# Performance work log

Hardware: AMD Instinct MI355X
Metric: run time of the kernel (lower is better)

Reference implementation:

```python
import jax, jax.numpy as jnp
import numpy as np

N, E, G = 50000, 600000, 512   # nodes, edges, graphs
F, D, L = 128, 128, 3          # in_features, hidden dim, num_gc_layers
ED = D * L                      # embedding_dim (readout='concat')
C = 1.0                         # curvature
MIN_NORM = 1e-15
BALL_EPS = 4e-3                 # hgcn PoincareBall proj eps for float32


def _logmap0(p, c):
    sc = jnp.sqrt(c)
    n = jnp.clip(jnp.linalg.norm(p, axis=-1, keepdims=True), MIN_NORM, None)
    return p / (sc * n) * jnp.arctanh(jnp.clip(sc * n, -1 + 1e-15, 1 - 1e-15))


def _expmap0(u, c):
    sc = jnp.sqrt(c)
    n = jnp.clip(jnp.linalg.norm(u, axis=-1, keepdims=True), MIN_NORM, None)
    return jnp.tanh(sc * n) * u / (sc * n)


def _proj(x, c):
    n = jnp.clip(jnp.linalg.norm(x, axis=-1, keepdims=True), MIN_NORM, None)
    maxn = (1.0 - BALL_EPS) / jnp.sqrt(c)
    return jnp.where(n > maxn, x / n * maxn, x)


def _gcn(x, W, b, src, dst):
    h = x @ W
    deg = jax.ops.segment_sum(jnp.ones_like(dst, dtype=h.dtype), dst, num_segments=N) + 1.0
    dinv = deg ** -0.5
    msg = h[src] * (dinv[src] * dinv[dst])[:, None]           # [E, D]
    agg = jax.ops.segment_sum(msg, dst, num_segments=N) + h * (dinv * dinv)[:, None]
    return agg + b


def _encoder(x, Ws, bs, src, dst, batch):
    xs = []
    for W, b in zip(Ws, bs):
        x = jax.nn.relu(_gcn(x, W, b, src, dst))
        xs.append(x)
    # readout='concat' with global_add_pool
    g = jnp.concatenate([jax.ops.segment_sum(h, batch, num_segments=G) for h in xs], axis=1)
    return g, jnp.concatenate(xs, axis=1)


def _mlp(x, W1, W2):  # proj_head: Linear (no bias), ReLU, Linear (no bias)
    return jax.nn.relu(x @ W1) @ W2


def setup_inputs() -> dict:
    key = jax.random.key(0)
    ks = jax.random.split(key, 24)

    def xav(k, i, o):
        return jax.random.normal(k, (i, o), dtype=jnp.float32) * np.float32(np.sqrt(2.0 / (i + o)))

    inp = {
        'x':   jax.random.normal(ks[0], (N, F), dtype=jnp.float32) * 1e-3,  # points inside the ball
        'x_s': jax.random.normal(ks[1], (N, F), dtype=jnp.float32) * 1e-3,
        'src': jax.random.randint(ks[2], (E,), 0, N, dtype=jnp.int32),
        'dst': jax.random.randint(ks[3], (E,), 0, N, dtype=jnp.int32),
        'batch': jnp.sort(jax.random.randint(ks[4], (N,), 0, G, dtype=jnp.int32)),
        # feature-branch GCN encoder
        'Wf0': xav(ks[5], F, D), 'Wf1': xav(ks[6], D, D), 'Wf2': xav(ks[7], D, D),
        'bf0': jnp.zeros((D,), jnp.float32), 'bf1': jnp.zeros((D,), jnp.float32), 'bf2': jnp.zeros((D,), jnp.float32),
        # structure-branch GCN encoder
        'Ws0': xav(ks[8], F, D), 'Ws1': xav(ks[9], D, D), 'Ws2': xav(ks[10], D, D),
        'bs0': jnp.zeros((D,), jnp.float32), 'bs1': jnp.zeros((D,), jnp.float32), 'bs2': jnp.zeros((D,), jnp.float32),
        # proj heads (biases removed by init_emb)
        'P1': xav(ks[11], ED, ED), 'P2': xav(ks[12], ED, ED),
        'G1': xav(ks[13], 2 * ED, ED), 'G2': xav(ks[14], ED, ED),
    }
    return inp


def reference(x, x_s, Wf0, Wf1, Wf2, bf0, bf1, bf2, Ws0, Ws1, Ws2, bs0, bs1, bs2, P1, P2, G1, G2, src, dst, batch):
    xt_f = _logmap0(x, C)
    xt_s = _logmap0(x_s, C)
    g_f, n_f = _encoder(xt_f, (Wf0, Wf1, Wf2), (bf0, bf1, bf2), src, dst, batch)
    g_s, n_s = _encoder(xt_s, (Ws0, Ws1, Ws2), (bs0, bs1, bs2), src, dst, batch)
    g = _mlp(jnp.concatenate((g_f, g_s), axis=1), G1, G2)
    e = lambda t: _proj(_expmap0(t, C), C)
    return (e(g), e(_mlp(g_f, P1, P2)), e(_mlp(n_f, P1, P2)), e(_mlp(g_s, P1, P2)), e(_mlp(n_s, P1, P2)))
```

## Files before the change

### kernel.cpp

```cpp
#include <hip/hip_runtime.h>
#include <math.h>

#define N_NODES 50000
#define N_EDGES 600000
#define N_GRAPHS 512
#define F_IN 128
#define D_HID 128
#define EDIM 384
#define M_ALL (N_NODES + N_GRAPHS)

typedef __attribute__((ext_vector_type(8))) short bf16x8;
typedef __attribute__((ext_vector_type(4))) float f32x4;
typedef __attribute__((ext_vector_type(16))) float f32x16;

static __device__ __forceinline__ float wave_reduce_sum(float s) {
#pragma unroll
  for (int off = 32; off > 0; off >>= 1) s += __shfl_xor(s, off, 64);
  return s;
}

static __device__ __forceinline__ int wave_reduce_sum_i(int s) {
#pragma unroll
  for (int off = 32; off > 0; off >>= 1) s += __shfl_xor(s, off, 64);
  return s;
}

static __device__ __forceinline__ short f2b(float f) {
  unsigned u = __float_as_uint(f);
  unsigned r = (u + 0x7FFFu + ((u >> 16) & 1u)) >> 16;
  return (short)r;
}

static __device__ __forceinline__ float b2f(short s) {
  return __uint_as_float(((unsigned)(unsigned short)s) << 16);
}


#define SCAN_BS 256
#define SCAN_NB ((N_NODES + SCAN_BS - 1) / SCAN_BS)

__global__ __launch_bounds__(SCAN_BS) void init_kernel(const int* __restrict__ batch,
                                                       int* __restrict__ cnt,
                                                       int* __restrict__ gptr) {
  int i = blockIdx.x * SCAN_BS + threadIdx.x;
  if (i < N_NODES) cnt[i] = 0;
  if (i <= N_GRAPHS) {
    int lo = 0, hi = N_NODES;
    while (lo < hi) { int mid = (lo + hi) >> 1; if (batch[mid] < i) lo = mid + 1; else hi = mid; }
    gptr[i] = lo;
  }
}

__global__ void hist_kernel(const int* __restrict__ dst, int* __restrict__ cnt) {
  int i = blockIdx.x * blockDim.x + threadIdx.x;
  if (i < N_EDGES) atomicAdd(&cnt[dst[i]], 1);
}

__global__ __launch_bounds__(SCAN_BS) void scan1_kernel(const int* __restrict__ cnt,
                                                        int* __restrict__ row_ptr,
                                                        int* __restrict__ bsum) {
  __shared__ int wsum[4];
  int tid = threadIdx.x, lane = tid & 63, wid = tid >> 6;
  int idx = blockIdx.x * SCAN_BS + tid;
  int v = (idx < N_NODES) ? cnt[idx] : 0;
  int x = v;
#pragma unroll
  for (int off = 1; off < 64; off <<= 1) {
    int t = __shfl_up(x, off, 64);
    if (lane >= off) x += t;
  }
  if (lane == 63) wsum[wid] = x;
  __syncthreads();
  int pre = 0, tot = 0;
#pragma unroll
  for (int w = 0; w < 4; ++w) { int s = wsum[w]; tot += s; if (w < wid) pre += s; }
  if (idx < N_NODES) row_ptr[idx + 1] = x + pre;
  if (tid == 0) bsum[blockIdx.x] = tot;
}

__global__ __launch_bounds__(SCAN_BS) void scan3_kernel(const int* __restrict__ cnt,
                                                        const int* __restrict__ bsum,
                                                        int* __restrict__ row_ptr,
                                                        int* __restrict__ cursor,
                                                        float* __restrict__ dinv) {
  __shared__ int ws[4];
  int tid = threadIdx.x, lane = tid & 63, wid = tid >> 6;
  int v = 0;
  if (tid < SCAN_NB && tid < blockIdx.x) v = bsum[tid];
  v = wave_reduce_sum_i(v);
  if (lane == 0) ws[wid] = v;
  __syncthreads();
  int boff = ws[0] + ws[1] + ws[2] + ws[3];
  int idx = blockIdx.x * SCAN_BS + tid;
  if (idx >= N_NODES) return;
  int val = row_ptr[idx + 1] + boff;
  row_ptr[idx + 1] = val;
  int c = cnt[idx];
  cursor[idx] = val - c;
  dinv[idx] = 1.0f / sqrtf((float)(c + 1));
  if (idx == 0) row_ptr[0] = 0;
}

__global__ void scatter_kernel(const int* __restrict__ src, const int* __restrict__ dst,
                               const float* __restrict__ dinv, int* __restrict__ cursor,
                               int* __restrict__ col, float* __restrict__ ew) {
  int e = blockIdx.x * blockDim.x + threadIdx.x;
  if (e >= N_EDGES) return;
  int s = src[e], d = dst[e];
  int pos = atomicAdd(&cursor[d], 1);
  col[pos] = s;
  ew[pos] = dinv[s] * dinv[d];
}


struct WcSeg { const float* W; short* Wt; int K; int Nc; };
struct WcArgs { WcSeg seg[10]; };

__global__ void wconv_all_kernel(WcArgs a) {
  int sidx = blockIdx.y;
  WcSeg s = a.seg[sidx];
  int i = blockIdx.x * blockDim.x + threadIdx.x;
  if (i >= s.K * s.Nc) return;
  int k = i / s.Nc, n = i - k * s.Nc;
  s.Wt[(size_t)n * s.K + k] = f2b(s.W[i]);
}


__global__ __launch_bounds__(256) void logmap2_kernel(const float* __restrict__ x,
                                                      const float* __restrict__ x_s,
                                                      short* __restrict__ Ab) {
  int w = blockIdx.x * 4 + (threadIdx.x >> 6);
  int lane = threadIdx.x & 63;
  if (w >= 2 * N_NODES) return;
  int br = (w >= N_NODES) ? 1 : 0;
  int row = br ? (w - N_NODES) : w;
  const float* xr = (br ? x_s : x) + (size_t)row * F_IN;
  float2 v = *(const float2*)(xr + lane * 2);
  float s = wave_reduce_sum(v.x * v.x + v.y * v.y);
  float n = sqrtf(s);
  float nc = fmaxf(n, 1e-15f);
  float f = atanhf(fminf(nc, 0.9999999f)) / nc;
  short2 o; o.x = f2b(v.x * f); o.y = f2b(v.y * f);
  *(short2*)(Ab + (size_t)row * 256 + br * 128 + lane * 2) = o;
}


__global__ __launch_bounds__(256) void agg2_kernel(const short* __restrict__ Xin, int lda,
                                                   const float* __restrict__ dinv,
                                                   const int* __restrict__ row_ptr,
                                                   const int* __restrict__ col,
                                                   const float* __restrict__ ew,
                                                   short* __restrict__ Xa) {
  int node = blockIdx.x * 4 + (threadIdx.x >> 6);
  int lane = threadIdx.x & 63;
  if (node >= N_NODES) return;
  float di = dinv[node];
  float wsf = di * di;
  short4 sv = *(const short4*)(Xin + (size_t)node * lda + lane * 4);
  float a0 = b2f(sv.x) * wsf, a1 = b2f(sv.y) * wsf, a2 = b2f(sv.z) * wsf, a3 = b2f(sv.w) * wsf;
  int s = row_ptr[node], e = row_ptr[node + 1];
  int j = s;
  for (; j + 4 <= e; j += 4) {
    int c0 = col[j], c1 = col[j + 1], c2 = col[j + 2], c3 = col[j + 3];
    float w0 = ew[j], w1 = ew[j + 1], w2 = ew[j + 2], w3 = ew[j + 3];
    short4 v0 = *(const short4*)(Xin + (size_t)c0 * lda + lane * 4);
    short4 v1 = *(const short4*)(Xin + (size_t)c1 * lda + lane * 4);
    short4 v2 = *(const short4*)(Xin + (size_t)c2 * lda + lane * 4);
    short4 v3 = *(const short4*)(Xin + (size_t)c3 * lda + lane * 4);
    a0 += b2f(v0.x) * w0; a1 += b2f(v0.y) * w0; a2 += b2f(v0.z) * w0; a3 += b2f(v0.w) * w0;
    a0 += b2f(v1.x) * w1; a1 += b2f(v1.y) * w1; a2 += b2f(v1.z) * w1; a3 += b2f(v1.w) * w1;
    a0 += b2f(v2.x) * w2; a1 += b2f(v2.y) * w2; a2 += b2f(v2.z) * w2; a3 += b2f(v2.w) * w2;
    a0 += b2f(v3.x) * w3; a1 += b2f(v3.y) * w3; a2 += b2f(v3.z) * w3; a3 += b2f(v3.w) * w3;
  }
  for (; j < e; ++j) {
    float w0 = ew[j];
    short4 v0 = *(const short4*)(Xin + (size_t)col[j] * lda + lane * 4);
    a0 += b2f(v0.x) * w0; a1 += b2f(v0.y) * w0; a2 += b2f(v0.z) * w0; a3 += b2f(v0.w) * w0;
  }
  short4 o; o.x = f2b(a0); o.y = f2b(a1); o.z = f2b(a2); o.w = f2b(a3);
  *(short4*)(Xa + (size_t)node * 256 + lane * 4) = o;
}


#define LDK 40

struct GemmZArgs {
  const short* A[2];
  const short* Bt[2];
  const float* bias[2];
  short* Cb[2];
  int lda, ldc, M, Nc, K, kexp, do_relu;
};

__global__ __launch_bounds__(256) void mfma_gemmz_kernel(GemmZArgs g) {
  __shared__ __align__(16) short As[128 * LDK];
  __shared__ __align__(16) short Bs[128 * LDK];
  int z = blockIdx.z;
  const short* __restrict__ A = g.A[z];
  const short* __restrict__ Bt = g.Bt[z];
  int tid = threadIdx.x;
  int wave = tid >> 6, lane = tid & 63;
  int wr = (wave >> 1) * 64, wc = (wave & 1) * 64;
  int q = lane >> 4, m = lane & 15;
  int row0 = blockIdx.x * 128, col0 = blockIdx.y * 128;
  f32x4 acc[4][4] = {};
  for (int k0 = 0; k0 < g.K; k0 += 32) {
#pragma unroll
    for (int p = 0; p < 2; ++p) {
      int idx = p * 256 + tid;
      int r = idx >> 2, kc = (idx & 3) * 8;
      int gr = row0 + r;
      int kk = k0 + kc;
      int acol = g.kexp ? (kk + ((kk >> 7) << 7)) : kk;
      float4 v = make_float4(0.f, 0.f, 0.f, 0.f);
      if (gr < g.M) v = *(const float4*)(A + (size_t)gr * g.lda + acol);
      *(float4*)(As + r * LDK + kc) = v;
      float4 w = *(const float4*)(Bt + (size_t)(col0 + r) * g.K + kk);
      *(float4*)(Bs + r * LDK + kc) = w;
    }
    __syncthreads();
    bf16x8 af[4], bfr[4];
#pragma unroll
    for (int i = 0; i < 4; ++i) {
      af[i]  = *(const bf16x8*)(As + (wr + i * 16 + m) * LDK + q * 8);
      bfr[i] = *(const bf16x8*)(Bs + (wc + i * 16 + m) * LDK + q * 8);
    }
#pragma unroll
    for (int i = 0; i < 4; ++i)
#pragma unroll
      for (int j = 0; j < 4; ++j)
        acc[i][j] = __builtin_amdgcn_mfma_f32_16x16x32_bf16(af[i], bfr[j], acc[i][j], 0, 0, 0);
    __syncthreads();
  }
  const float* __restrict__ bias = g.bias[z];
  short* __restrict__ Cb = g.Cb[z];
#pragma unroll
  for (int i = 0; i < 4; ++i) {
#pragma unroll
    for (int r = 0; r < 4; ++r) {
      int rr = row0 + wr + i * 16 + q * 4 + r;
      if (rr >= g.M) continue;
#pragma unroll
      for (int j = 0; j < 4; ++j) {
        int cc = col0 + wc + j * 16 + m;
        float v = acc[i][j][r];
        if (bias) v += bias[cc];
        if (g.do_relu) v = fmaxf(v, 0.0f);
        Cb[(size_t)rr * g.ldc + cc] = f2b(v);
      }
    }
  }
}


#define HLD 392

struct MlpProb {
  const short* A;
  const short* B1;
  const short* B2;
  float* Cf;
  float* Cf2;
  int lda, M, K1, kexp, split;
};
struct Mlp2Args { MlpProb p[3]; int gx_h; };

__global__ __launch_bounds__(512) void mlp2_kernel(Mlp2Args g) {
  __shared__ __align__(16) short As[128 * LDK];
  __shared__ __align__(16) short Bs[384 * LDK];
  __shared__ __align__(16) short H[128 * HLD];
  __shared__ float nsum[128][4];
  int z = blockIdx.z;
  int bx = blockIdx.x;
  MlpProb p;
  int row0;
  if (bx < g.gx_h) { p = g.p[z]; row0 = bx * 128; }
  else { if (z) return; p = g.p[2]; row0 = (bx - g.gx_h) * 128; }

  int tid = threadIdx.x;
  int wave = tid >> 6, lane = tid & 63;
  int l31 = lane & 31, lh = lane >> 5;
  int rg = wave & 1;
  int cq = wave >> 1;

  int r_a = tid >> 2, kc_a = (tid & 3) * 8;

  auto loadA1 = [&](int k0) {
    int gr = row0 + r_a;
    int kk = k0 + kc_a;
    int acol = p.kexp ? (kk + ((kk >> 7) << 7)) : kk;
    float4 v = make_float4(0.f, 0.f, 0.f, 0.f);
    if (gr < p.M) v = *(const float4*)(p.A + (size_t)gr * p.lda + acol);
    return v;
  };

  f32x16 acc[2][3] = {};
  float4 pa, pb0, pb1, pb2;
  pa = loadA1(0);
  pb0 = *(const float4*)(p.B1 + (size_t)(0 * 128 + r_a) * p.K1 + kc_a);
  pb1 = *(const float4*)(p.B1 + (size_t)(1 * 128 + r_a) * p.K1 + kc_a);
  pb2 = *(const float4*)(p.B1 + (size_t)(2 * 128 + r_a) * p.K1 + kc_a);

  for (int k0 = 0; k0 < p.K1; k0 += 32) {
    *(float4*)(As + r_a * LDK + kc_a) = pa;
    *(float4*)(Bs + (0 * 128 + r_a) * LDK + kc_a) = pb0;
    *(float4*)(Bs + (1 * 128 + r_a) * LDK + kc_a) = pb1;
    *(float4*)(Bs + (2 * 128 + r_a) * LDK + kc_a) = pb2;
    int kn = k0 + 32;
    if (kn < p.K1) {
      pa = loadA1(kn);
      pb0 = *(const float4*)(p.B1 + (size_t)(0 * 128 + r_a) * p.K1 + kn + kc_a);
      pb1 = *(const float4*)(p.B1 + (size_t)(1 * 128 + r_a) * p.K1 + kn + kc_a);
      pb2 = *(const float4*)(p.B1 + (size_t)(2 * 128 + r_a) * p.K1 + kn + kc_a);
    } else {
      pb0 = *(const float4*)(p.B2 + (size_t)(0 * 128 + r_a) * 384 + kc_a);
      pb1 = *(const float4*)(p.B2 + (size_t)(1 * 128 + r_a) * 384 + kc_a);
      pb2 = *(const float4*)(p.B2 + (size_t)(2 * 128 + r_a) * 384 + kc_a);
    }
    asm volatile("s_waitcnt lgkmcnt(0)" ::: "memory");
    __builtin_amdgcn_sched_barrier(0);
    __builtin_amdgcn_s_barrier();
#pragma unroll
    for (int ks = 0; ks < 32; ks += 16) {
      int kloc = ks + lh * 8;
      bf16x8 a0 = *(const bf16x8*)(As + (rg * 64 + l31) * LDK + kloc);
      bf16x8 a1 = *(const bf16x8*)(As + (rg * 64 + 32 + l31) * LDK + kloc);
      bf16x8 b0 = *(const bf16x8*)(Bs + (cq * 96 + l31) * LDK + kloc);
      bf16x8 b1 = *(const bf16x8*)(Bs + (cq * 96 + 32 + l31) * LDK + kloc);
      bf16x8 b2 = *(const bf16x8*)(Bs + (cq * 96 + 64 + l31) * LDK + kloc);
      acc[0][0] = __builtin_amdgcn_mfma_f32_32x32x16_bf16(a0, b0, acc[0][0], 0, 0, 0);
      acc[1][0] = __builtin_amdgcn_mfma_f32_32x32x16_bf16(a1, b0, acc[1][0], 0, 0, 0);
      acc[0][1] = __builtin_amdgcn_mfma_f32_32x32x16_bf16(a0, b1, acc[0][1], 0, 0, 0);
      acc[1][1] = __builtin_amdgcn_mfma_f32_32x32x16_bf16(a1, b1, acc[1][1], 0, 0, 0);
      acc[0][2] = __builtin_amdgcn_mfma_f32_32x32x16_bf16(a0, b2, acc[0][2], 0, 0, 0);
      acc[1][2] = __builtin_amdgcn_mfma_f32_32x32x16_bf16(a1, b2, acc[1][2], 0, 0, 0);
    }
    __builtin_amdgcn_s_barrier();
  }
#pragma unroll
  for (int rf = 0; rf < 2; ++rf)
#pragma unroll
    for (int f = 0; f < 3; ++f)
#pragma unroll
      for (int reg = 0; reg < 16; ++reg) {
        int rl = rg * 64 + rf * 32 + (reg & 3) + 8 * (reg >> 2) + 4 * lh;
        H[rl * HLD + cq * 96 + f * 32 + l31] = f2b(fmaxf(acc[rf][f][reg], 0.0f));
      }
#pragma unroll
  for (int rf = 0; rf < 2; ++rf)
#pragma unroll
    for (int f = 0; f < 3; ++f) acc[rf][f] = (f32x16){};
  asm volatile("s_waitcnt lgkmcnt(0)" ::: "memory");
  __builtin_amdgcn_sched_barrier(0);
  __builtin_amdgcn_s_barrier();
  for (int k0 = 0; k0 < 384; k0 += 32) {
    *(float4*)(Bs + (0 * 128 + r_a) * LDK + kc_a) = pb0;
    *(float4*)(Bs + (1 * 128 + r_a) * LDK + kc_a) = pb1;
    *(float4*)(Bs + (2 * 128 + r_a) * LDK + kc_a) = pb2;
    int kn = k0 + 32;
    if (kn < 384) {
      pb0 = *(const float4*)(p.B2 + (size_t)(0 * 128 + r_a) * 384 + kn + kc_a);
      pb1 = *(const float4*)(p.B2 + (size_t)(1 * 128 + r_a) * 384 + kn + kc_a);
      pb2 = *(const float4*)(p.B2 + (size_t)(2 * 128 + r_a) * 384 + kn + kc_a);
    }
    asm volatile("s_waitcnt lgkmcnt(0)" ::: "memory");
    __builtin_amdgcn_sched_barrier(0);
    __builtin_amdgcn_s_barrier();
#pragma unroll
    for (int ks = 0; ks < 32; ks += 16) {
      int kloc = ks + lh * 8;
      bf16x8 a0 = *(const bf16x8*)(H + (rg * 64 + l31) * HLD + k0 + kloc);
      bf16x8 a1 = *(const bf16x8*)(H + (rg * 64 + 32 + l31) * HLD + k0 + kloc);
      bf16x8 b0 = *(const bf16x8*)(Bs + (cq * 96 + l31) * LDK + kloc);
      bf16x8 b1 = *(const bf16x8*)(Bs + (cq * 96 + 32 + l31) * LDK + kloc);
      bf16x8 b2 = *(const bf16x8*)(Bs + (cq * 96 + 64 + l31) * LDK + kloc);
      acc[0][0] = __builtin_amdgcn_mfma_f32_32x32x16_bf16(a0, b0, acc[0][0], 0, 0, 0);
      acc[1][0] = __builtin_amdgcn_mfma_f32_32x32x16_bf16(a1, b0, acc[1][0], 0, 0, 0);
      acc[0][1] = __builtin_amdgcn_mfma_f32_32x32x16_bf16(a0, b1, acc[0][1], 0, 0, 0);
      acc[1][1] = __builtin_amdgcn_mfma_f32_32x32x16_bf16(a1, b1, acc[1][1], 0, 0, 0);
      acc[0][2] = __builtin_amdgcn_mfma_f32_32x32x16_bf16(a0, b2, acc[0][2], 0, 0, 0);
      acc[1][2] = __builtin_amdgcn_mfma_f32_32x32x16_bf16(a1, b2, acc[1][2], 0, 0, 0);
    }
    __builtin_amdgcn_s_barrier();
  }
#pragma unroll
  for (int rf = 0; rf < 2; ++rf)
#pragma unroll
    for (int reg = 0; reg < 16; ++reg) {
      float s = acc[rf][0][reg] * acc[rf][0][reg] + acc[rf][1][reg] * acc[rf][1][reg] +
                acc[rf][2][reg] * acc[rf][2][reg];
      s += __shfl_xor(s, 1, 64);
      s += __shfl_xor(s, 2, 64);
      s += __shfl_xor(s, 4, 64);
      s += __shfl_xor(s, 8, 64);
      s += __shfl_xor(s, 16, 64);
      if (l31 == 0)
        nsum[rg * 64 + rf * 32 + (reg & 3) + 8 * (reg >> 2) + 4 * lh][cq] = s;
    }
  __syncthreads();
  const float maxn = 1.0f - 4e-3f;
#pragma unroll
  for (int rf = 0; rf < 2; ++rf)
#pragma unroll
    for (int reg = 0; reg < 16; ++reg) {
      int rl = rg * 64 + rf * 32 + (reg & 3) + 8 * (reg >> 2) + 4 * lh;
      int rr = row0 + rl;
      if (rr >= p.M) continue;
      float s = nsum[rl][0] + nsum[rl][1] + nsum[rl][2] + nsum[rl][3];
      float n = fmaxf(sqrtf(s), 1e-15f);
      float th = tanhf(n);
      float fct = th / n;
      float n2 = fmaxf(th, 1e-15f);
      if (n2 > maxn) fct *= maxn / n2;
      float* base = (rr < p.split) ? (p.Cf + (size_t)rr * 384)
                                   : (p.Cf2 + (size_t)(rr - p.split) * 384);
#pragma unroll
      for (int f = 0; f < 3; ++f)
        base[cq * 96 + f * 32 + l31] = acc[rf][f][reg] * fct;
    }
}


__global__ __launch_bounds__(768) void pool2_kernel(const short* __restrict__ NB,
                                                    const int* __restrict__ gptr,
                                                    short* __restrict__ GCb,
                                                    short* __restrict__ nbappend) {
  int g = blockIdx.x, t = threadIdx.x;
  int s = gptr[g], e = gptr[g + 1];
  float acc = 0.0f;
  for (int i = s; i < e; ++i) acc += b2f(NB[(size_t)i * 768 + t]);
  short bv = f2b(acc);
  int l = t >> 8, rem = t & 255, b = rem >> 7, c = rem & 127;
  GCb[(size_t)g * 768 + b * 384 + l * 128 + c] = bv;
  nbappend[(size_t)g * 768 + t] = bv;
}


extern "C" void kernel_launch(void* const* d_in, const int* in_sizes, int n_in,
                              void* d_out, int out_size, void* d_ws, size_t ws_size,
                              hipStream_t stream) {
  (void)in_sizes; (void)n_in; (void)out_size; (void)ws_size;
  const float* x   = (const float*)d_in[0];
  const float* x_s = (const float*)d_in[1];
  const int* src   = (const int*)d_in[2];
  const int* dst   = (const int*)d_in[3];
  const int* batch = (const int*)d_in[4];
  const float* Wf[3] = {(const float*)d_in[5], (const float*)d_in[6], (const float*)d_in[7]};
  const float* bf[3] = {(const float*)d_in[8], (const float*)d_in[9], (const float*)d_in[10]};
  const float* Wsb[3] = {(const float*)d_in[11], (const float*)d_in[12], (const float*)d_in[13]};
  const float* bs[3] = {(const float*)d_in[14], (const float*)d_in[15], (const float*)d_in[16]};
  const float* P1 = (const float*)d_in[17];
  const float* P2 = (const float*)d_in[18];
  const float* G1 = (const float*)d_in[19];
  const float* G2 = (const float*)d_in[20];
  float* out = (float*)d_out;

  char* w = (char*)d_ws;
  auto alloc = [&](size_t bytes) {
    char* p = w;
    w += (bytes + 255) & ~(size_t)255;
    return p;
  };
  short* Ab    = (short*)alloc((size_t)N_NODES * 256 * 2);
  short* Xa    = (short*)alloc((size_t)N_NODES * 256 * 2);
  short* NB    = (short*)alloc((size_t)M_ALL * 768 * 2);
  int* cnt     = (int*)alloc((size_t)N_NODES * 4);
  int* row_ptr = (int*)alloc((size_t)(N_NODES + 1) * 4);
  int* cursor  = (int*)alloc((size_t)N_NODES * 4);
  float* dinv  = (float*)alloc((size_t)N_NODES * 4);
  int* col     = (int*)alloc((size_t)N_EDGES * 4);
  float* ew    = (float*)alloc((size_t)N_EDGES * 4);
  int* gptr    = (int*)alloc((size_t)(N_GRAPHS + 1) * 4);
  int* bsum    = (int*)alloc(256 * 4);
  short* GCb   = (short*)alloc((size_t)N_GRAPHS * 768 * 2);
  short* P1t   = (short*)alloc((size_t)EDIM * EDIM * 2);
  short* P2t   = (short*)alloc((size_t)EDIM * EDIM * 2);
  short* G1t   = (short*)alloc((size_t)768 * EDIM * 2);
  short* G2t   = (short*)alloc((size_t)EDIM * EDIM * 2);
  short* Wft[3], *Wst[3];
  for (int l = 0; l < 3; ++l) {
    Wft[l] = (short*)alloc((size_t)128 * 128 * 2);
    Wst[l] = (short*)alloc((size_t)128 * 128 * 2);
  }

  {
    WcArgs wa;
    wa.seg[0] = {P1, P1t, EDIM, EDIM};
    wa.seg[1] = {P2, P2t, EDIM, EDIM};
    wa.seg[2] = {G1, G1t, 768, EDIM};
    wa.seg[3] = {G2, G2t, EDIM, EDIM};
    for (int l = 0; l < 3; ++l) {
      wa.seg[4 + l] = {Wf[l], Wft[l], 128, 128};
      wa.seg[7 + l] = {Wsb[l], Wst[l], 128, 128};
    }
    wconv_all_kernel<<<dim3((768 * EDIM + 255) / 256, 10), 256, 0, stream>>>(wa);
  }

  init_kernel<<<SCAN_NB, SCAN_BS, 0, stream>>>(batch, cnt, gptr);
  hist_kernel<<<(N_EDGES + 255) / 256, 256, 0, stream>>>(dst, cnt);
  scan1_kernel<<<SCAN_NB, SCAN_BS, 0, stream>>>(cnt, row_ptr, bsum);
  scan3_kernel<<<SCAN_NB, SCAN_BS, 0, stream>>>(cnt, bsum, row_ptr, cursor, dinv);
  scatter_kernel<<<(N_EDGES + 255) / 256, 256, 0, stream>>>(src, dst, dinv, cursor, col, ew);

  const size_t OUT0 = 0;
  const size_t OUT1 = (size_t)N_GRAPHS * EDIM;
  const size_t OUT2 = OUT1 + (size_t)N_GRAPHS * EDIM;
  const size_t OUT3 = OUT2 + (size_t)N_NODES * EDIM;

  const int gx_layer = (N_NODES + 127) / 128;
  const int gx_mfma  = (M_ALL + 127) / 128;
  const int gx_agg   = (N_NODES + 3) / 4;

  logmap2_kernel<<<(2 * N_NODES + 3) / 4, 256, 0, stream>>>(x, x_s, Ab);

  const short* cur = Ab;
  int clda = 256;
  for (int l = 0; l < 3; ++l) {
    agg2_kernel<<<gx_agg, 256, 0, stream>>>(cur, clda, dinv, row_ptr, col, ew, Xa);
    GemmZArgs ga = {};
    ga.A[0] = Xa;        ga.A[1] = Xa + 128;
    ga.Bt[0] = Wft[l];   ga.Bt[1] = Wst[l];
    ga.bias[0] = bf[l];  ga.bias[1] = bs[l];
    ga.Cb[0] = NB + l * 256;        ga.Cb[1] = NB + l * 256 + 128;
    ga.lda = 256; ga.ldc = 768; ga.M = N_NODES; ga.Nc = 128; ga.K = 128;
    ga.kexp = 0; ga.do_relu = 1;
    mfma_gemmz_kernel<<<dim3(gx_layer, 1, 2), 256, 0, stream>>>(ga);
    cur = NB + l * 256;
    clda = 768;
  }

  pool2_kernel<<<N_GRAPHS, 768, 0, stream>>>(NB, gptr, GCb, NB + (size_t)N_NODES * 768);

  {
    const int gx_g = (N_GRAPHS + 127) / 128;
    Mlp2Args h = {};
    h.p[0] = {NB,       P1t, P2t, out + OUT2,
              out + OUT1, 768, M_ALL, EDIM, 1, N_NODES};
    h.p[1] = {NB + 128, P1t, P2t, out + OUT3 + (size_t)N_GRAPHS * EDIM,
              out + OUT3, 768, M_ALL, EDIM, 1, N_NODES};
    h.p[2] = {GCb, G1t, G2t, out + OUT0, out + OUT0, 768, N_GRAPHS, 768, 0, 1 << 30};
    h.gx_h = gx_mfma;
    mlp2_kernel<<<dim3(gx_mfma + gx_g, 1, 2), 512, 0, stream>>>(h);
  }
}
```

Measured before the change: 720.3 us.

## Fuse GCN neighbor aggregation with the per-layer MFMA GEMM via LDS

Merges the separate aggregation kernel and the two-branch GEMM into one kernel per layer. Each block aggregates 64 nodes into shared memory, then multiplies them by both branch weight matrices using 32x32x16 MFMA and writes bias+ReLU output directly. This removes the Xa intermediate round-trip through global memory and one launch per layer. In exchange, blocks are larger and serialize gather then compute, so occupancy and latency hiding during the irregular gather may drop.

```diff
diff --git a/kernel.cpp b/kernel.cpp
--- a/kernel.cpp
+++ b/kernel.cpp
@@ -145,111 +145,100 @@
 }
 
 
-__global__ __launch_bounds__(256) void agg2_kernel(const short* __restrict__ Xin, int lda,
-                                                   const float* __restrict__ dinv,
-                                                   const int* __restrict__ row_ptr,
-                                                   const int* __restrict__ col,
-                                                   const float* __restrict__ ew,
-                                                   short* __restrict__ Xa) {
-  int node = blockIdx.x * 4 + (threadIdx.x >> 6);
-  int lane = threadIdx.x & 63;
-  if (node >= N_NODES) return;
-  float di = dinv[node];
-  float wsf = di * di;
-  short4 sv = *(const short4*)(Xin + (size_t)node * lda + lane * 4);
-  float a0 = b2f(sv.x) * wsf, a1 = b2f(sv.y) * wsf, a2 = b2f(sv.z) * wsf, a3 = b2f(sv.w) * wsf;
-  int s = row_ptr[node], e = row_ptr[node + 1];
-  int j = s;
-  for (; j + 4 <= e; j += 4) {
-    int c0 = col[j], c1 = col[j + 1], c2 = col[j + 2], c3 = col[j + 3];
-    float w0 = ew[j], w1 = ew[j + 1], w2 = ew[j + 2], w3 = ew[j + 3];
-    short4 v0 = *(const short4*)(Xin + (size_t)c0 * lda + lane * 4);
-    short4 v1 = *(const short4*)(Xin + (size_t)c1 * lda + lane * 4);
-    short4 v2 = *(const short4*)(Xin + (size_t)c2 * lda + lane * 4);
-    short4 v3 = *(const short4*)(Xin + (size_t)c3 * lda + lane * 4);
-    a0 += b2f(v0.x) * w0; a1 += b2f(v0.y) * w0; a2 += b2f(v0.z) * w0; a3 += b2f(v0.w) * w0;
-    a0 += b2f(v1.x) * w1; a1 += b2f(v1.y) * w1; a2 += b2f(v1.z) * w1; a3 += b2f(v1.w) * w1;
-    a0 += b2f(v2.x) * w2; a1 += b2f(v2.y) * w2; a2 += b2f(v2.z) * w2; a3 += b2f(v2.w) * w2;
-    a0 += b2f(v3.x) * w3; a1 += b2f(v3.y) * w3; a2 += b2f(v3.z) * w3; a3 += b2f(v3.w) * w3;
-  }
-  for (; j < e; ++j) {
-    float w0 = ew[j];
-    short4 v0 = *(const short4*)(Xin + (size_t)col[j] * lda + lane * 4);
-    a0 += b2f(v0.x) * w0; a1 += b2f(v0.y) * w0; a2 += b2f(v0.z) * w0; a3 += b2f(v0.w) * w0;
-  }
-  short4 o; o.x = f2b(a0); o.y = f2b(a1); o.z = f2b(a2); o.w = f2b(a3);
-  *(short4*)(Xa + (size_t)node * 256 + lane * 4) = o;
-}
-
-
 #define LDK 40
-
-struct GemmZArgs {
-  const short* A[2];
-  const short* Bt[2];
+#define XLD 264
+
+struct AggGemmArgs {
+  const short* Xin;
+  const float* dinv;
+  const int* row_ptr;
+  const int* col;
+  const float* ew;
+  const short* Wt[2];
   const float* bias[2];
-  short* Cb[2];
-  int lda, ldc, M, Nc, K, kexp, do_relu;
+  short* outNB;
+  int lda;
 };
 
-__global__ __launch_bounds__(256) void mfma_gemmz_kernel(GemmZArgs g) {
-  __shared__ __align__(16) short As[128 * LDK];
-  __shared__ __align__(16) short Bs[128 * LDK];
-  int z = blockIdx.z;
-  const short* __restrict__ A = g.A[z];
-  const short* __restrict__ Bt = g.Bt[z];
+__global__ __launch_bounds__(256) void agg_gemm_kernel(AggGemmArgs g) {
+  __shared__ __align__(16) short Xs[64 * XLD];
+  __shared__ __align__(16) short Bs[256 * LDK];
   int tid = threadIdx.x;
   int wave = tid >> 6, lane = tid & 63;
-  int wr = (wave >> 1) * 64, wc = (wave & 1) * 64;
-  int q = lane >> 4, m = lane & 15;
-  int row0 = blockIdx.x * 128, col0 = blockIdx.y * 128;
-  f32x4 acc[4][4] = {};
-  for (int k0 = 0; k0 < g.K; k0 += 32) {
-#pragma unroll
-    for (int p = 0; p < 2; ++p) {
+  int n0 = blockIdx.x * 64;
+  for (int i = 0; i < 16; ++i) {
+    int lrow = wave * 16 + i;
+    int node = n0 + lrow;
+    if (node >= N_NODES) break;
+    float di = g.dinv[node];
+    float wsf = di * di;
+    short4 sv = *(const short4*)(g.Xin + (size_t)node * g.lda + lane * 4);
+    float a0 = b2f(sv.x) * wsf, a1 = b2f(sv.y) * wsf, a2 = b2f(sv.z) * wsf,
+          a3 = b2f(sv.w) * wsf;
+    int s = g.row_ptr[node], e = g.row_ptr[node + 1];
+    int j = s;
+    for (; j + 4 <= e; j += 4) {
+      int c0 = g.col[j], c1 = g.col[j + 1], c2 = g.col[j + 2], c3 = g.col[j + 3];
+      float w0 = g.ew[j], w1 = g.ew[j + 1], w2 = g.ew[j + 2], w3 = g.ew[j + 3];
+      short4 v0 = *(const short4*)(g.Xin + (size_t)c0 * g.lda + lane * 4);
+      short4 v1 = *(const short4*)(g.Xin + (size_t)c1 * g.lda + lane * 4);
+      short4 v2 = *(const short4*)(g.Xin + (size_t)c2 * g.lda + lane * 4);
+      short4 v3 = *(const short4*)(g.Xin + (size_t)c3 * g.lda + lane * 4);
+      a0 += b2f(v0.x) * w0; a1 += b2f(v0.y) * w0; a2 += b2f(v0.z) * w0; a3 += b2f(v0.w) * w0;
+      a0 += b2f(v1.x) * w1; a1 += b2f(v1.y) * w1; a2 += b2f(v1.z) * w1; a3 += b2f(v1.w) * w1;
+      a0 += b2f(v2.x) * w2; a1 += b2f(v2.y) * w2; a2 += b2f(v2.z) * w2; a3 += b2f(v2.w) * w2;
+      a0 += b2f(v3.x) * w3; a1 += b2f(v3.y) * w3; a2 += b2f(v3.z) * w3; a3 += b2f(v3.w) * w3;
+    }
+    for (; j < e; ++j) {
+      float w0 = g.ew[j];
+      short4 v0 = *(const short4*)(g.Xin + (size_t)g.col[j] * g.lda + lane * 4);
+      a0 += b2f(v0.x) * w0; a1 += b2f(v0.y) * w0; a2 += b2f(v0.z) * w0; a3 += b2f(v0.w) * w0;
+    }
+    short4 o; o.x = f2b(a0); o.y = f2b(a1); o.z = f2b(a2); o.w = f2b(a3);
+    *(short4*)(Xs + lrow * XLD + lane * 4) = o;
+  }
+  __syncthreads();
+  int l31 = lane & 31, lh = lane >> 5;
+  int rg = wave & 1, b = wave >> 1;
+  f32x16 acc[4] = {};
+  for (int k0 = 0; k0 < 128; k0 += 32) {
+#pragma unroll
+    for (int p = 0; p < 4; ++p) {
       int idx = p * 256 + tid;
-      int r = idx >> 2, kc = (idx & 3) * 8;
-      int gr = row0 + r;
-      int kk = k0 + kc;
-      int acol = g.kexp ? (kk + ((kk >> 7) << 7)) : kk;
-      float4 v = make_float4(0.f, 0.f, 0.f, 0.f);
-      if (gr < g.M) v = *(const float4*)(A + (size_t)gr * g.lda + acol);
-      *(float4*)(As + r * LDK + kc) = v;
-      float4 w = *(const float4*)(Bt + (size_t)(col0 + r) * g.K + kk);
-      *(float4*)(Bs + r * LDK + kc) = w;
+      int br = idx >> 9;
+      int rem = idx & 511;
+      int r = rem >> 2, kc = (rem & 3) * 8;
+      float4 w0 = *(const float4*)(g.Wt[br] + (size_t)r * 128 + k0 + kc);
+      *(float4*)(Bs + (br * 128 + r) * LDK + kc) = w0;
     }
     __syncthreads();
-    bf16x8 af[4], bfr[4];
-#pragma unroll
-    for (int i = 0; i < 4; ++i) {
-      af[i]  = *(const bf16x8*)(As + (wr + i * 16 + m) * LDK + q * 8);
-      bfr[i] = *(const bf16x8*)(Bs + (wc + i * 16 + m) * LDK + q * 8);
-    }
-#pragma unroll
-    for (int i = 0; i < 4; ++i)
-#pragma unroll
-      for (int j = 0; j < 4; ++j)
-        acc[i][j] = __builtin_amdgcn_mfma_f32_16x16x32_bf16(af[i], bfr[j], acc[i][j], 0, 0, 0);
+#pragma unroll
+    for (int ks = 0; ks < 32; ks += 16) {
+      int kl = ks + lh * 8;
+      bf16x8 a = *(const bf16x8*)(Xs + (rg * 32 + l31) * XLD + b * 128 + k0 + kl);
+      bf16x8 b0 = *(const bf16x8*)(Bs + (b * 128 + 0 * 32 + l31) * LDK + kl);
+      bf16x8 b1 = *(const bf16x8*)(Bs + (b * 128 + 1 * 32 + l31) * LDK + kl);
+      bf16x8 b2 = *(const bf16x8*)(Bs + (b * 128 + 2 * 32 + l31) * LDK + kl);
+      bf16x8 b3 = *(const bf16x8*)(Bs + (b * 128 + 3 * 32 + l31) * LDK + kl);
+      acc[0] = __builtin_amdgcn_mfma_f32_32x32x16_bf16(a, b0, acc[0], 0, 0, 0);
+      acc[1] = __builtin_amdgcn_mfma_f32_32x32x16_bf16(a, b1, acc[1], 0, 0, 0);
+      acc[2] = __builtin_amdgcn_mfma_f32_32x32x16_bf16(a, b2, acc[2], 0, 0, 0);
+      acc[3] = __builtin_amdgcn_mfma_f32_32x32x16_bf16(a, b3, acc[3], 0, 0, 0);
+    }
     __syncthreads();
   }
-  const float* __restrict__ bias = g.bias[z];
-  short* __restrict__ Cb = g.Cb[z];
-#pragma unroll
-  for (int i = 0; i < 4; ++i) {
-#pragma unroll
-    for (int r = 0; r < 4; ++r) {
-      int rr = row0 + wr + i * 16 + q * 4 + r;
-      if (rr >= g.M) continue;
-#pragma unroll
-      for (int j = 0; j < 4; ++j) {
-        int cc = col0 + wc + j * 16 + m;
-        float v = acc[i][j][r];
-        if (bias) v += bias[cc];
-        if (g.do_relu) v = fmaxf(v, 0.0f);
-        Cb[(size_t)rr * g.ldc + cc] = f2b(v);
-      }
-    }
-  }
+  const float* bb = g.bias[b];
+#pragma unroll
+  for (int cf = 0; cf < 4; ++cf)
+#pragma unroll
+    for (int reg = 0; reg < 16; ++reg) {
+      int row = rg * 32 + (reg & 3) + 8 * (reg >> 2) + 4 * lh;
+      int node = n0 + row;
+      if (node >= N_NODES) continue;
+      float v = acc[cf][reg] + bb[cf * 32 + l31];
+      v = fmaxf(v, 0.0f);
+      g.outNB[(size_t)node * 768 + b * 128 + cf * 32 + l31] = f2b(v);
+    }
 }
 
 
@@ -462,7 +451,6 @@
     return p;
   };
   short* Ab    = (short*)alloc((size_t)N_NODES * 256 * 2);
-  short* Xa    = (short*)alloc((size_t)N_NODES * 256 * 2);
   short* NB    = (short*)alloc((size_t)M_ALL * 768 * 2);
   int* cnt     = (int*)alloc((size_t)N_NODES * 4);
   int* row_ptr = (int*)alloc((size_t)(N_NODES + 1) * 4);
@@ -507,24 +495,21 @@
   const size_t OUT2 = OUT1 + (size_t)N_GRAPHS * EDIM;
   const size_t OUT3 = OUT2 + (size_t)N_NODES * EDIM;
 
-  const int gx_layer = (N_NODES + 127) / 128;
-  const int gx_mfma  = (M_ALL + 127) / 128;
-  const int gx_agg   = (N_NODES + 3) / 4;
+  const int gx_mfma = (M_ALL + 127) / 128;
+  const int gx_ag   = (N_NODES + 63) / 64;
 
   logmap2_kernel<<<(2 * N_NODES + 3) / 4, 256, 0, stream>>>(x, x_s, Ab);
 
   const short* cur = Ab;
   int clda = 256;
   for (int l = 0; l < 3; ++l) {
-    agg2_kernel<<<gx_agg, 256, 0, stream>>>(cur, clda, dinv, row_ptr, col, ew, Xa);
-    GemmZArgs ga = {};
-    ga.A[0] = Xa;        ga.A[1] = Xa + 128;
-    ga.Bt[0] = Wft[l];   ga.Bt[1] = Wst[l];
-    ga.bias[0] = bf[l];  ga.bias[1] = bs[l];
-    ga.Cb[0] = NB + l * 256;        ga.Cb[1] = NB + l * 256 + 128;
-    ga.lda = 256; ga.ldc = 768; ga.M = N_NODES; ga.Nc = 128; ga.K = 128;
-    ga.kexp = 0; ga.do_relu = 1;
-    mfma_gemmz_kernel<<<dim3(gx_layer, 1, 2), 256, 0, stream>>>(ga);
+    AggGemmArgs ga = {};
+    ga.Xin = cur; ga.dinv = dinv; ga.row_ptr = row_ptr; ga.col = col; ga.ew = ew;
+    ga.Wt[0] = Wft[l]; ga.Wt[1] = Wst[l];
+    ga.bias[0] = bf[l]; ga.bias[1] = bs[l];
+    ga.outNB = NB + l * 256;
+    ga.lda = clda;
+    agg_gemm_kernel<<<gx_ag, 256, 0, stream>>>(ga);
     cur = NB + l * 256;
     clda = 768;
   }
```

Result: slower. 887.3 us (+23.2%).
